# Optimization experiments

Hardware: AMD Instinct MI355X
Metric: run time of the kernel (lower is better)

The kernel has to match this reference:

```python
import jax, jax.numpy as jnp
import numpy as np

D = 256      # model dim
H = 4        # heads
L = 6        # layers (shared weights)
N = 32768    # neuron dim; per-head hidden = N//H = 8192
VOCAB = 256
B, T = 2, 2048
EPS = 1e-5


def _ln(x):
    # LayerNorm over last dim, no affine (matches nn.LayerNorm(D, elementwise_affine=False))
    m = jnp.mean(x, axis=-1, keepdims=True)
    v = jnp.mean((x - m) ** 2, axis=-1, keepdims=True)
    return (x - m) * jax.lax.rsqrt(v + EPS)


def _rope(x):
    # x: [B, H, T, d]
    d = x.shape[-1]
    t = x.shape[-2]
    inv_freq = 1.0 / (10000.0 ** (jnp.arange(0, d, 2, dtype=jnp.float32) / d))
    freqs = jnp.arange(t, dtype=jnp.float32)[:, None] * inv_freq[None, :]  # [T, d/2]
    emb = jnp.concatenate([freqs, freqs], axis=-1)                          # [T, d]
    x1, x2 = x[..., : d // 2], x[..., d // 2 :]
    x_rot = jnp.concatenate([-x2, x1], axis=-1)
    return x * jnp.cos(emb) + x_rot * jnp.sin(emb)


def _linear_attn(q, k, v):
    # q,k: [B,H,T,n]; v: [B,T,D]. Raw (unnormalized) scores, STRICTLY causal mask
    # (tril with diagonal=-1, i.e. token t attends to s < t only), no softmax.
    qr = _rope(q)
    kr = _rope(k)
    scores = jnp.einsum('bhtn,bhsn->bhts', qr, kr)  # [B,H,T,T]
    t_idx = jnp.arange(q.shape[-2])
    mask = t_idx[:, None] > t_idx[None, :]          # strict lower triangle
    scores = jnp.where(mask, scores, jnp.zeros((), scores.dtype))
    return jnp.einsum('bhts,bsd->bhtd', scores, v)  # [B,H,T,D]


def setup_inputs() -> dict:
    key = jax.random.key(0)
    ks = jax.random.split(key, 6)
    idx = jax.random.randint(ks[0], (B, T), 0, VOCAB, dtype=jnp.int64)
    std = 0.02
    wte = std * jax.random.normal(ks[1], (VOCAB, D), dtype=jnp.float32)
    encoder = std * jax.random.normal(ks[2], (N, D), dtype=jnp.float32)
    decoder_x = std * jax.random.normal(ks[3], (H, D, N // H), dtype=jnp.float32)
    decoder_y = std * jax.random.normal(ks[4], (H, D, N // H), dtype=jnp.float32)
    readout = std * jax.random.normal(ks[5], (D, VOCAB), dtype=jnp.float32)
    return {"idx": idx, "wte": wte, "encoder": encoder,
            "decoder_x": decoder_x, "decoder_y": decoder_y, "readout": readout}


def reference(idx, wte, encoder, decoder_x, decoder_y, readout):
    # Dropout is identity in eval mode.
    v_ast = _ln(wte[idx])  # [B,T,D]
    for _ in range(L):  # weights SHARED across layers
        x = jax.nn.relu(jnp.einsum('btd,hdn->bhtn', v_ast, decoder_x))  # [B,H,T,N/H]
        a_ast = _linear_attn(x, x, v_ast)                               # [B,H,T,D]
        y = jax.nn.relu(jnp.einsum('bhtd,hdn->bhtn', _ln(a_ast), decoder_y)) * x
        y_flat = jnp.transpose(y, (0, 2, 1, 3)).reshape(y.shape[0], y.shape[2], N)  # [B,T,N]
        v_ast = _ln(v_ast + _ln(y_flat @ encoder))
    return v_ast @ readout  # [B,T,VOCAB]
```

## Files before the change

### kernel.cpp

```cpp
#include <hip/hip_runtime.h>
#include <stdint.h>

typedef unsigned short u16;
typedef __bf16 bfv8 __attribute__((ext_vector_type(8)));
typedef float f32x4 __attribute__((ext_vector_type(4)));

#define BM 128
#define BN 128
#define BK 32

__device__ __forceinline__ float b2f(u16 u){ union{float f; unsigned int i;} x; x.i = ((unsigned int)u)<<16; return x.f; }
__device__ __forceinline__ u16 f2b(float f){ union{float f; unsigned int i;} x; x.f = f; unsigned int r = x.i + 0x7fffu + ((x.i>>16)&1u); return (u16)(r>>16); }

__device__ __forceinline__ void load16_lds(const void* g, void* l){
  __builtin_amdgcn_global_load_lds(
      (const __attribute__((address_space(1))) void*)g,
      (__attribute__((address_space(3))) void*)l, 16, 0, 0);
}

__device__ __forceinline__ void swz(int& bx, int& by, int& bz){
  int gx = gridDim.x, gy = gridDim.y;
  int nw = gx*gy*gridDim.z;
  int flat = blockIdx.x + gx*(blockIdx.y + gy*blockIdx.z);
  int q = nw >> 3, r = nw & 7, xcd = flat & 7, i = flat >> 3;
  int wg = (xcd < r ? xcd*(q+1) : r*(q+1) + (xcd-r)*q) + i;
  bx = wg % gx; int t = wg / gx; by = t % gy; bz = t / gy;
}

struct GP {
  const u16* A; const u16* Bt; const u16* A2; const u16* Bt2;
  const u16* ct; const u16* st;
  float* Cf; u16* Cb; u16* Y;
  int bh0, zs, zm;
};

template<int LDA, int LDB, bool PAIRB>
__device__ __forceinline__ void kloop(const u16* A, const u16* Bt, int m0, int n0,
                                      int kbeg, int kend,
                                      u16 (&As)[2][4096], u16 (&Bs)[2][4096],
                                      f32x4 (&acc)[4][4]){
  const int tid = threadIdx.x;
  const int lane = tid & 63;
  const int wid = tid >> 6;
  const int wm = wid >> 1, wn = wid & 1;
  const int srow = tid >> 2, sslot = tid & 3;
  const int nt = (kend - kbeg) / BK;
  if (nt <= 0) return;

  auto stage = [&](int k0, int buf){
    #pragma unroll
    for (int q = 0; q < 2; ++q){
      int row = q*64 + srow;
      int ks = sslot ^ ((row >> 1) & 3);
      load16_lds(A + (long)(m0 + row)*LDA + (k0 + ks*8), &As[buf][q*2048 + wid*512]);
    }
    #pragma unroll
    for (int q = 0; q < 2; ++q){
      int row = q*64 + srow;
      int ks = sslot ^ ((row >> 1) & 3);
      long brow;
      if (PAIRB){ int wnb = row >> 6, sub = (row >> 5) & 1, r5 = row & 31;
                  brow = n0 + wnb*32 + r5 + sub*4096; }
      else brow = n0 + row;
      load16_lds(Bt + brow*(long)LDB + (k0 + ks*8), &Bs[buf][q*2048 + wid*512]);
    }
  };

  stage(kbeg, 0);
  int cur = 0;
  for (int t = 0; t < nt; ++t){
    int tn = (t+1 < nt) ? (t+1) : t;
    stage(kbeg + tn*BK, cur^1);
    asm volatile("s_waitcnt vmcnt(4)" ::: "memory");
    __builtin_amdgcn_s_barrier();
    bfv8 af[4], bf[4];
    const int r16 = lane & 15, s4 = lane >> 4;
    #pragma unroll
    for (int i = 0; i < 4; ++i){
      int ar = wm*64 + i*16 + r16;
      af[i] = *(const bfv8*)(&As[cur][ar*BK + ((s4 ^ ((ar>>1)&3))*8)]);
      int br = wn*64 + i*16 + r16;
      bf[i] = *(const bfv8*)(&Bs[cur][br*BK + ((s4 ^ ((br>>1)&3))*8)]);
    }
    #pragma unroll
    for (int i = 0; i < 4; ++i)
      #pragma unroll
      for (int j = 0; j < 4; ++j)
        acc[i][j] = __builtin_amdgcn_mfma_f32_16x16x32_bf16(af[i], bf[j], acc[i][j], 0,0,0);
    asm volatile("s_waitcnt lgkmcnt(0)" ::: "memory");
    __builtin_amdgcn_s_barrier();
    cur ^= 1;
  }
  asm volatile("s_waitcnt vmcnt(0)" ::: "memory");
  __builtin_amdgcn_s_barrier();
}

#define EPI_SETUP const int lane = threadIdx.x & 63, wid = threadIdx.x >> 6; \
  const int wm = wid >> 1, wn = wid & 1; const int r16 = lane & 15, s4 = lane >> 4;

__global__ __launch_bounds__(256) void g_rope(GP p){
  int bx, by, bz; swz(bx, by, bz);
  const int m0 = by*BM, n0 = bx*64, z = bz;
  const int bh = p.bh0 + z, b = bh >> 2, h = bh & 3;
  __shared__ u16 As[2][4096], Bs[2][4096];
  f32x4 acc[4][4] = {};
  kloop<256,256,true>(p.A + (long)b*524288, p.Bt + (long)h*2097152, m0, n0, 0, 256, As, Bs, acc);
  EPI_SETUP
  #pragma unroll
  for (int i = 0; i < 4; ++i)
    #pragma unroll
    for (int j = 0; j < 2; ++j){
      int cl = n0 + wn*32 + j*16 + r16;
      #pragma unroll
      for (int v = 0; v < 4; ++v){
        int row = m0 + wm*64 + i*16 + s4*4 + v;
        float x1 = fmaxf(acc[i][j][v], 0.f);
        float x2 = fmaxf(acc[i][j+2][v], 0.f);
        float c = b2f(p.ct[(long)row*4096 + cl]);
        float s = b2f(p.st[(long)row*4096 + cl]);
        p.Cb[(long)z*16777216 + (long)row*8192 + cl]        = f2b(x1*c - x2*s);
        p.Cb[(long)z*16777216 + (long)row*8192 + cl + 4096] = f2b(x2*c + x1*s);
      }
    }
}

__global__ __launch_bounds__(256) void g_qk(GP p){
  int bx, by, bz; swz(bx, by, bz);
  const int m0 = by*BM, n0 = bx*BN, z = bz;
  if (n0 >= m0 + BM) return;
  __shared__ u16 As[2][4096], Bs[2][4096];
  f32x4 acc[4][4] = {};
  const u16* A = p.A + (long)z*16777216;
  kloop<8192,8192,false>(A, A, m0, n0, 0, 8192, As, Bs, acc);
  EPI_SETUP
  #pragma unroll
  for (int i = 0; i < 4; ++i)
    #pragma unroll
    for (int j = 0; j < 4; ++j){
      int col = n0 + wn*64 + j*16 + r16;
      #pragma unroll
      for (int v = 0; v < 4; ++v){
        int row = m0 + wm*64 + i*16 + s4*4 + v;
        p.Cb[(long)z*4194304 + (long)row*2048 + col] = f2b(row > col ? acc[i][j][v] : 0.f);
      }
    }
}

__global__ __launch_bounds__(256) void g_pv(GP p){
  int bx, by, bz; swz(bx, by, bz);
  const int m0 = by*BM, n0 = bx*BN;
  const int head = bz >> p.zs, sl = bz & p.zm;
  const int b = (p.bh0 + head) >> 2;
  const int kc = 2048 >> p.zs;
  const int kbeg = sl*kc;
  const int kend = min(min(2048, m0 + BM), kbeg + kc);
  __shared__ u16 As[2][4096], Bs[2][4096];
  f32x4 acc[4][4] = {};
  kloop<2048,2048,false>(p.A + (long)head*4194304, p.Bt + (long)b*524288, m0, n0, kbeg, kend, As, Bs, acc);
  EPI_SETUP
  #pragma unroll
  for (int i = 0; i < 4; ++i)
    #pragma unroll
    for (int j = 0; j < 4; ++j){
      int col = n0 + wn*64 + j*16 + r16;
      #pragma unroll
      for (int v = 0; v < 4; ++v){
        int row = m0 + wm*64 + i*16 + s4*4 + v;
        p.Cf[(long)bz*524288 + (long)row*256 + col] = acc[i][j][v];
      }
    }
}

__global__ __launch_bounds__(256) void g_fuse(GP p){
  int bx, by, bz; swz(bx, by, bz);
  const int m0 = by*BM, n0 = bx*BN, z = bz;
  const int bh = p.bh0 + z, b = bh >> 2, h = bh & 3;
  __shared__ u16 As[2][4096], Bs[2][4096];
  f32x4 acc1[4][4] = {}, acc2[4][4] = {};
  kloop<256,256,false>(p.A  + (long)z*524288, p.Bt  + (long)h*2097152, m0, n0, 0, 256, As, Bs, acc1);
  kloop<256,256,false>(p.A2 + (long)b*524288, p.Bt2 + (long)h*2097152, m0, n0, 0, 256, As, Bs, acc2);
  EPI_SETUP
  #pragma unroll
  for (int i = 0; i < 4; ++i)
    #pragma unroll
    for (int j = 0; j < 4; ++j){
      int col = n0 + wn*64 + j*16 + r16;
      #pragma unroll
      for (int v = 0; v < 4; ++v){
        int row = m0 + wm*64 + i*16 + s4*4 + v;
        p.Y[(long)z*16777216 + (long)row*8192 + col] =
            f2b(fmaxf(acc1[i][j][v], 0.f) * fmaxf(acc2[i][j][v], 0.f));
      }
    }
}

__global__ __launch_bounds__(256) void g_enc(GP p){
  int bx, by, bz; swz(bx, by, bz);
  const int m0 = by*BM, n0 = bx*BN;
  const int head = bz >> p.zs, sp = bz & p.zm;
  const int h = (p.bh0 + head) & 3;
  const int kc = 8192 >> p.zs;
  const int kbeg = sp*kc, kend = kbeg + kc;
  __shared__ u16 As[2][4096], Bs[2][4096];
  f32x4 acc[4][4] = {};
  kloop<8192,32768,false>(p.A + (long)head*16777216, p.Bt + (long)h*8192, m0, n0, kbeg, kend, As, Bs, acc);
  EPI_SETUP
  #pragma unroll
  for (int i = 0; i < 4; ++i)
    #pragma unroll
    for (int j = 0; j < 4; ++j){
      int col = n0 + wn*64 + j*16 + r16;
      #pragma unroll
      for (int v = 0; v < 4; ++v){
        int row = m0 + wm*64 + i*16 + s4*4 + v;
        p.Cf[(long)bz*524288 + (long)row*256 + col] = acc[i][j][v];
      }
    }
}

__global__ __launch_bounds__(256) void g_out(GP p){
  int bx, by, bz; swz(bx, by, bz); (void)bz;
  const int m0 = by*BM, n0 = bx*BN;
  __shared__ u16 As[2][4096], Bs[2][4096];
  f32x4 acc[4][4] = {};
  kloop<256,256,false>(p.A, p.Bt, m0, n0, 0, 256, As, Bs, acc);
  EPI_SETUP
  #pragma unroll
  for (int i = 0; i < 4; ++i)
    #pragma unroll
    for (int j = 0; j < 4; ++j){
      int col = n0 + wn*64 + j*16 + r16;
      #pragma unroll
      for (int v = 0; v < 4; ++v){
        int row = m0 + wm*64 + i*16 + s4*4 + v;
        p.Cf[(long)row*256 + col] = acc[i][j][v];
      }
    }
}


__device__ __forceinline__ float wave_sum(float v){
  #pragma unroll
  for (int o = 32; o > 0; o >>= 1) v += __shfl_down(v, o, 64);
  return v;
}
__device__ __forceinline__ float block_sum(float v, float* sm){
  v = wave_sum(v);
  __syncthreads();
  if ((threadIdx.x & 63) == 0) sm[threadIdx.x >> 6] = v;
  __syncthreads();
  return sm[0] + sm[1] + sm[2] + sm[3];
}

__global__ __launch_bounds__(256) void k_embed(const int* idx, const float* wte,
                                               float* v, u16* vbf, u16* vbt){
  __shared__ float sm[4];
  __shared__ int is64_s;
  int row = blockIdx.x, d = threadIdx.x;
  int oddnz = (d < 64) ? (idx[2*d + 1] != 0) : 0;
  unsigned long long mb = __ballot(oddnz);
  if (threadIdx.x == 0) is64_s = (mb == 0ULL);
  __syncthreads();
  int tok = is64_s ? idx[2*row] : idx[row];
  float x = wte[tok*256 + d];
  float m = block_sum(x, sm) * (1.f/256.f);
  float dd = x - m;
  float var = block_sum(dd*dd, sm) * (1.f/256.f);
  float y = dd * rsqrtf(var + 1e-5f);
  v[(long)row*256 + d] = y;
  vbf[(long)row*256 + d] = f2b(y);
  int b = row >> 11, t = row & 2047;
  vbt[((long)(b*256 + d))*2048 + t] = f2b(y);
}

__global__ __launch_bounds__(256) void k_ln(const float* abuf, u16* out, int pv){
  __shared__ float sm[4];
  int row = blockIdx.x, d = threadIdx.x;
  int head = row >> 11, t = row & 2047;
  float x = 0.f;
  for (int s = 0; s < pv; ++s) x += abuf[((long)(head*pv + s) << 19) + (long)t*256 + d];
  float m = block_sum(x, sm) * (1.f/256.f);
  float dd = x - m;
  float var = block_sum(dd*dd, sm) * (1.f/256.f);
  out[(long)row*256 + d] = f2b(dd * rsqrtf(var + 1e-5f));
}

__global__ __launch_bounds__(256) void k_acc(const float* part, float* t1,
                                             int bh0, int gc, int ps){
  int t = blockIdx.x, d = threadIdx.x;
  long o = (long)t*256 + d;
  float s0 = 0.f, s1 = 0.f;
  for (int z = 0; z < gc; ++z){
    float v = 0.f;
    for (int sp = 0; sp < ps; ++sp) v += part[((long)(z*ps + sp) << 19) + o];
    if (((bh0 + z) >> 2) == 0) s0 += v; else s1 += v;
  }
  #pragma unroll
  for (int b = 0; b < 2; ++b){
    int lo = bh0 > 4*b ? bh0 : 4*b;
    int hi = (bh0 + gc) < (4*b + 4) ? (bh0 + gc) : (4*b + 4);
    if (lo < hi){
      float s = b == 0 ? s0 : s1;
      if (lo == 4*b) t1[((long)b << 19) + o] = s;
      else           t1[((long)b << 19) + o] += s;
    }
  }
}

__global__ __launch_bounds__(256) void k_finish(const float* t1, float* v, u16* vbf, u16* vbt){
  __shared__ float sm[4];
  int row = blockIdx.x; int d = threadIdx.x;
  int b = row >> 11, t = row & 2047;
  float s = t1[(long)row*256 + d];
  float m = block_sum(s, sm) * (1.f/256.f);
  float dd = s - m;
  float var = block_sum(dd*dd, sm) * (1.f/256.f);
  float u = dd * rsqrtf(var + 1e-5f);
  float wv = v[(long)row*256 + d] + u;
  float m2 = block_sum(wv, sm) * (1.f/256.f);
  float d2 = wv - m2;
  float v2 = block_sum(d2*d2, sm) * (1.f/256.f);
  float y = d2 * rsqrtf(v2 + 1e-5f);
  v[(long)row*256 + d] = y;
  vbf[(long)row*256 + d] = f2b(y);
  vbt[((long)(b*256 + d))*2048 + t] = f2b(y);
}

__global__ __launch_bounds__(256) void k_cossin(u16* ct, u16* st){
  int tid = blockIdx.x*256 + threadIdx.x;
  int t = tid >> 12, i = tid & 4095;
  float f = powf(10000.0f, -(float)i * (1.0f/4096.0f));
  float a = (float)t * f;
  float s, c; sincosf(a, &s, &c);
  ct[tid] = f2b(c); st[tid] = f2b(s);
}

__global__ void k_transpose(const float* in, u16* out, int R, int C, long in_z, long out_z){
  __shared__ float tile[32][33];
  const float* I = in + (long)blockIdx.z * in_z;
  u16* O = out + (long)blockIdx.z * out_z;
  int c0 = blockIdx.x*32, r0 = blockIdx.y*32;
  int tx = threadIdx.x, ty = threadIdx.y;
  #pragma unroll
  for (int k = 0; k < 4; ++k){ int r = ty + k*8; tile[r][tx] = I[(long)(r0+r)*C + c0+tx]; }
  __syncthreads();
  #pragma unroll
  for (int k = 0; k < 4; ++k){ int r = ty + k*8; O[(long)(c0+r)*R + r0+tx] = f2b(tile[tx][r]); }
}


extern "C" void kernel_launch(void* const* d_in, const int* in_sizes, int n_in,
                              void* d_out, int out_size, void* d_ws, size_t ws_size,
                              hipStream_t stream){
  const int*   idx = (const int*)d_in[0];
  const float* wte = (const float*)d_in[1];
  const float* enc = (const float*)d_in[2];
  const float* dx  = (const float*)d_in[3];
  const float* dy  = (const float*)d_in[4];
  const float* ro  = (const float*)d_in[5];
  float* out = (float*)d_out;
  (void)in_sizes; (void)n_in; (void)out_size;

  const size_t base_b = 96600064UL;
  struct Cfg { int gc, pvs, pss; };
  const Cfg lad[] = {{8,2,3},{4,2,3},{2,2,3},{2,1,2},{1,2,3},{1,1,2},{1,0,1},{1,0,0}};
  Cfg cfg = lad[7];
  for (int i = 0; i < 8; ++i){
    size_t ch = (size_t)lad[i].gc * (33554432UL + 8388608UL + 1048576UL
               + ((size_t)(1 << lad[i].pvs))*2097152UL
               + ((size_t)(1 << lad[i].pss))*2097152UL);
    if (base_b + ch <= ws_size){ cfg = lad[i]; break; }
  }
  const int gc = cfg.gc, pvs = cfg.pvs, pss = cfg.pss;
  const int pv = 1 << pvs, ps = 1 << pss;

  char* w = (char*)d_ws;
  size_t off = 0;
  auto alloc = [&](size_t b){ size_t r = off; off += (b + 255) & ~(size_t)255; return r; };
  float* v_ast = (float*)(w + alloc(4096UL*256*4));
  u16*   v_bf  = (u16*)  (w + alloc(4096UL*256*2));
  u16*   v_bt  = (u16*)  (w + alloc(2UL*256*2048*2));
  u16*   dxT   = (u16*)  (w + alloc(4UL*8192*256*2));
  u16*   dyT   = (u16*)  (w + alloc(4UL*8192*256*2));
  u16*   encT  = (u16*)  (w + alloc(256UL*32768*2));
  u16*   roT   = (u16*)  (w + alloc(256UL*256*2));
  u16*   ct    = (u16*)  (w + alloc(2048UL*4096*2));
  u16*   st    = (u16*)  (w + alloc(2048UL*4096*2));
  float* t1    = (float*)(w + alloc(2UL*2048*256*4));
  u16*   xbuf  = (u16*)  (w + alloc((size_t)gc*33554432));
  u16*   scb   = (u16*)  (w + alloc((size_t)gc*8388608));
  u16*   lnAb  = (u16*)  (w + alloc((size_t)gc*1048576));
  float* abuf  = (float*)(w + alloc((size_t)gc*pv*2097152UL));
  float* part  = (float*)(w + alloc((size_t)gc*ps*2097152UL));

  dim3 tb(32, 8);
  k_cossin<<<32768, 256, 0, stream>>>(ct, st);
  k_transpose<<<dim3(256, 8, 4),  tb, 0, stream>>>(dx,  dxT,  256,   8192, 256L*8192, 8192L*256);
  k_transpose<<<dim3(256, 8, 4),  tb, 0, stream>>>(dy,  dyT,  256,   8192, 256L*8192, 8192L*256);
  k_transpose<<<dim3(8, 1024, 1), tb, 0, stream>>>(enc, encT, 32768, 256,  0, 0);
  k_transpose<<<dim3(8, 8, 1),    tb, 0, stream>>>(ro,  roT,  256,   256,  0, 0);
  k_embed<<<4096, 256, 0, stream>>>(idx, wte, v_ast, v_bf, v_bt);

  for (int l = 0; l < 6; ++l){
    for (int bh0 = 0; bh0 < 8; bh0 += gc){
      { GP g{}; g.bh0=bh0; g.A=v_bf; g.Bt=dxT; g.ct=ct; g.st=st; g.Cb=xbuf;
        g_rope<<<dim3(64,16,gc), 256, 0, stream>>>(g); }
      { GP g{}; g.bh0=bh0; g.A=xbuf; g.Cb=scb;
        g_qk<<<dim3(16,16,gc), 256, 0, stream>>>(g); }
      { GP g{}; g.bh0=bh0; g.A=scb; g.Bt=v_bt; g.Cf=abuf; g.zs=pvs; g.zm=pv-1;
        g_pv<<<dim3(2,16,gc*pv), 256, 0, stream>>>(g); }
      k_ln<<<gc*2048, 256, 0, stream>>>(abuf, lnAb, pv);
      { GP g{}; g.bh0=bh0; g.A=lnAb; g.Bt=dyT; g.A2=v_bf; g.Bt2=dxT; g.Y=xbuf;
        g_fuse<<<dim3(64,16,gc), 256, 0, stream>>>(g); }
      { GP g{}; g.bh0=bh0; g.A=xbuf; g.Bt=encT; g.Cf=part; g.zs=pss; g.zm=ps-1;
        g_enc<<<dim3(2,16,gc*ps), 256, 0, stream>>>(g); }
      k_acc<<<2048, 256, 0, stream>>>(part, t1, bh0, gc, ps);
    }
    k_finish<<<4096, 256, 0, stream>>>(t1, v_ast, v_bf, v_bt);
  }
  { GP g{}; g.A=v_bf; g.Bt=roT; g.Cf=out;
    g_out<<<dim3(2,32,1), 256, 0, stream>>>(g); }
}
```

Measured before the change: 7.998 ms.

## Shrink workspace via buffer aliasing so more heads fit per group

Drops the fp32 residual copy and keeps the residual only in bf16, which adds rounding error to the residual path. Partial-sum and LayerNorm buffers are aliased onto the score buffer, and the readout transpose reuses t1 after the layer loop. The smaller footprint lets more (batch, head) pairs be processed per group, with g_enc and g_pv split factors fixed lower and a ragged last group handled. The GEMM k-loop is also peeled so the final tile is no longer staged redundantly.

After: 8.165 ms. +2.1%, slower.

```diff
diff --git a/kernel.cpp b/kernel.cpp
--- a/kernel.cpp
+++ b/kernel.cpp
@@ -65,34 +65,39 @@
       load16_lds(Bt + brow*(long)LDB + (k0 + ks*8), &Bs[buf][q*2048 + wid*512]);
     }
   };
+  auto compute = [&](int buf){
+    bfv8 af[4], bf[4];
+    const int r16 = lane & 15, s4 = lane >> 4;
+    #pragma unroll
+    for (int i = 0; i < 4; ++i){
+      int ar = wm*64 + i*16 + r16;
+      af[i] = *(const bfv8*)(&As[buf][ar*BK + ((s4 ^ ((ar>>1)&3))*8)]);
+      int br = wn*64 + i*16 + r16;
+      bf[i] = *(const bfv8*)(&Bs[buf][br*BK + ((s4 ^ ((br>>1)&3))*8)]);
+    }
+    #pragma unroll
+    for (int i = 0; i < 4; ++i)
+      #pragma unroll
+      for (int j = 0; j < 4; ++j)
+        acc[i][j] = __builtin_amdgcn_mfma_f32_16x16x32_bf16(af[i], bf[j], acc[i][j], 0,0,0);
+  };
 
   stage(kbeg, 0);
   int cur = 0;
-  for (int t = 0; t < nt; ++t){
-    int tn = (t+1 < nt) ? (t+1) : t;
-    stage(kbeg + tn*BK, cur^1);
+  for (int t = 0; t < nt-1; ++t){
+    stage(kbeg + (t+1)*BK, cur^1);
     asm volatile("s_waitcnt vmcnt(4)" ::: "memory");
     __builtin_amdgcn_s_barrier();
-    bfv8 af[4], bf[4];
-    const int r16 = lane & 15, s4 = lane >> 4;
-    #pragma unroll
-    for (int i = 0; i < 4; ++i){
-      int ar = wm*64 + i*16 + r16;
-      af[i] = *(const bfv8*)(&As[cur][ar*BK + ((s4 ^ ((ar>>1)&3))*8)]);
-      int br = wn*64 + i*16 + r16;
-      bf[i] = *(const bfv8*)(&Bs[cur][br*BK + ((s4 ^ ((br>>1)&3))*8)]);
-    }
-    #pragma unroll
-    for (int i = 0; i < 4; ++i)
-      #pragma unroll
-      for (int j = 0; j < 4; ++j)
-        acc[i][j] = __builtin_amdgcn_mfma_f32_16x16x32_bf16(af[i], bf[j], acc[i][j], 0,0,0);
+    compute(cur);
     asm volatile("s_waitcnt lgkmcnt(0)" ::: "memory");
     __builtin_amdgcn_s_barrier();
     cur ^= 1;
   }
   asm volatile("s_waitcnt vmcnt(0)" ::: "memory");
   __builtin_amdgcn_s_barrier();
+  compute(cur);
+  asm volatile("s_waitcnt lgkmcnt(0)" ::: "memory");
+  __builtin_amdgcn_s_barrier();
 }
 
 #define EPI_SETUP const int lane = threadIdx.x & 63, wid = threadIdx.x >> 6; \
@@ -133,6 +138,7 @@
   const u16* A = p.A + (long)z*16777216;
   kloop<8192,8192,false>(A, A, m0, n0, 0, 8192, As, Bs, acc);
   EPI_SETUP
+  u16* C = p.Cb + (long)z*4194304;
   #pragma unroll
   for (int i = 0; i < 4; ++i)
     #pragma unroll
@@ -141,7 +147,7 @@
       #pragma unroll
       for (int v = 0; v < 4; ++v){
         int row = m0 + wm*64 + i*16 + s4*4 + v;
-        p.Cb[(long)z*4194304 + (long)row*2048 + col] = f2b(row > col ? acc[i][j][v] : 0.f);
+        C[(long)row*2048 + col] = f2b(row > col ? acc[i][j][v] : 0.f);
       }
     }
 }
@@ -253,7 +259,7 @@
 }
 
 __global__ __launch_bounds__(256) void k_embed(const int* idx, const float* wte,
-                                               float* v, u16* vbf, u16* vbt){
+                                               u16* vbf, u16* vbt){
   __shared__ float sm[4];
   __shared__ int is64_s;
   int row = blockIdx.x, d = threadIdx.x;
@@ -267,7 +273,6 @@
   float dd = x - m;
   float var = block_sum(dd*dd, sm) * (1.f/256.f);
   float y = dd * rsqrtf(var + 1e-5f);
-  v[(long)row*256 + d] = y;
   vbf[(long)row*256 + d] = f2b(y);
   int b = row >> 11, t = row & 2047;
   vbt[((long)(b*256 + d))*2048 + t] = f2b(y);
@@ -307,7 +312,7 @@
   }
 }
 
-__global__ __launch_bounds__(256) void k_finish(const float* t1, float* v, u16* vbf, u16* vbt){
+__global__ __launch_bounds__(256) void k_finish(const float* t1, u16* vbf, u16* vbt){
   __shared__ float sm[4];
   int row = blockIdx.x; int d = threadIdx.x;
   int b = row >> 11, t = row & 2047;
@@ -316,12 +321,11 @@
   float dd = s - m;
   float var = block_sum(dd*dd, sm) * (1.f/256.f);
   float u = dd * rsqrtf(var + 1e-5f);
-  float wv = v[(long)row*256 + d] + u;
+  float wv = b2f(vbf[(long)row*256 + d]) + u;
   float m2 = block_sum(wv, sm) * (1.f/256.f);
   float d2 = wv - m2;
   float v2 = block_sum(d2*d2, sm) * (1.f/256.f);
   float y = d2 * rsqrtf(v2 + 1e-5f);
-  v[(long)row*256 + d] = y;
   vbf[(long)row*256 + d] = f2b(y);
   vbt[((long)(b*256 + d))*2048 + t] = f2b(y);
 }
@@ -361,63 +365,62 @@
   float* out = (float*)d_out;
   (void)in_sizes; (void)n_in; (void)out_size;
 
-  const size_t base_b = 96600064UL;
-  struct Cfg { int gc, pvs, pss; };
-  const Cfg lad[] = {{8,2,3},{4,2,3},{2,2,3},{2,1,2},{1,2,3},{1,1,2},{1,0,1},{1,0,0}};
-  Cfg cfg = lad[7];
-  for (int i = 0; i < 8; ++i){
-    size_t ch = (size_t)lad[i].gc * (33554432UL + 8388608UL + 1048576UL
-               + ((size_t)(1 << lad[i].pvs))*2097152UL
-               + ((size_t)(1 << lad[i].pss))*2097152UL);
-    if (base_b + ch <= ws_size){ cfg = lad[i]; break; }
+  int gc = 1, pv = 2;
+  {
+    const int gcs[4] = {4, 3, 2, 1};
+    for (int i = 0; i < 4; ++i){
+      int g = gcs[i]; int pvt = (g >= 4) ? 1 : 2;
+      size_t need = 92274688UL + (size_t)g*(33554432UL + 8388608UL + (size_t)pvt*2097152UL);
+      if (need <= ws_size){ gc = g; pv = pvt; break; }
+    }
   }
-  const int gc = cfg.gc, pvs = cfg.pvs, pss = cfg.pss;
-  const int pv = 1 << pvs, ps = 1 << pss;
+  const int ps = 2;
+  const int pvs = (pv == 2) ? 1 : 0;
 
   char* w = (char*)d_ws;
   size_t off = 0;
   auto alloc = [&](size_t b){ size_t r = off; off += (b + 255) & ~(size_t)255; return r; };
-  float* v_ast = (float*)(w + alloc(4096UL*256*4));
   u16*   v_bf  = (u16*)  (w + alloc(4096UL*256*2));
   u16*   v_bt  = (u16*)  (w + alloc(2UL*256*2048*2));
   u16*   dxT   = (u16*)  (w + alloc(4UL*8192*256*2));
   u16*   dyT   = (u16*)  (w + alloc(4UL*8192*256*2));
   u16*   encT  = (u16*)  (w + alloc(256UL*32768*2));
-  u16*   roT   = (u16*)  (w + alloc(256UL*256*2));
   u16*   ct    = (u16*)  (w + alloc(2048UL*4096*2));
   u16*   st    = (u16*)  (w + alloc(2048UL*4096*2));
   float* t1    = (float*)(w + alloc(2UL*2048*256*4));
   u16*   xbuf  = (u16*)  (w + alloc((size_t)gc*33554432));
   u16*   scb   = (u16*)  (w + alloc((size_t)gc*8388608));
-  u16*   lnAb  = (u16*)  (w + alloc((size_t)gc*1048576));
   float* abuf  = (float*)(w + alloc((size_t)gc*pv*2097152UL));
-  float* part  = (float*)(w + alloc((size_t)gc*ps*2097152UL));
+  float* part  = (float*)scb;
+  u16*   lnAb  = (u16*)((char*)scb + (size_t)gc*ps*2097152UL);
+  u16*   roT   = (u16*)t1;
 
   dim3 tb(32, 8);
   k_cossin<<<32768, 256, 0, stream>>>(ct, st);
   k_transpose<<<dim3(256, 8, 4),  tb, 0, stream>>>(dx,  dxT,  256,   8192, 256L*8192, 8192L*256);
   k_transpose<<<dim3(256, 8, 4),  tb, 0, stream>>>(dy,  dyT,  256,   8192, 256L*8192, 8192L*256);
   k_transpose<<<dim3(8, 1024, 1), tb, 0, stream>>>(enc, encT, 32768, 256,  0, 0);
-  k_transpose<<<dim3(8, 8, 1),    tb, 0, stream>>>(ro,  roT,  256,   256,  0, 0);
-  k_embed<<<4096, 256, 0, stream>>>(idx, wte, v_ast, v_bf, v_bt);
+  k_embed<<<4096, 256, 0, stream>>>(idx, wte, v_bf, v_bt);
 
   for (int l = 0; l < 6; ++l){
     for (int bh0 = 0; bh0 < 8; bh0 += gc){
+      int ze = (8 - bh0 < gc) ? (8 - bh0) : gc;
       { GP g{}; g.bh0=bh0; g.A=v_bf; g.Bt=dxT; g.ct=ct; g.st=st; g.Cb=xbuf;
-        g_rope<<<dim3(64,16,gc), 256, 0, stream>>>(g); }
+        g_rope<<<dim3(64,16,ze), 256, 0, stream>>>(g); }
       { GP g{}; g.bh0=bh0; g.A=xbuf; g.Cb=scb;
-        g_qk<<<dim3(16,16,gc), 256, 0, stream>>>(g); }
+        g_qk<<<dim3(16,16,ze), 256, 0, stream>>>(g); }
       { GP g{}; g.bh0=bh0; g.A=scb; g.Bt=v_bt; g.Cf=abuf; g.zs=pvs; g.zm=pv-1;
-        g_pv<<<dim3(2,16,gc*pv), 256, 0, stream>>>(g); }
-      k_ln<<<gc*2048, 256, 0, stream>>>(abuf, lnAb, pv);
+        g_pv<<<dim3(2,16,ze*pv), 256, 0, stream>>>(g); }
+      k_ln<<<ze*2048, 256, 0, stream>>>(abuf, lnAb, pv);
       { GP g{}; g.bh0=bh0; g.A=lnAb; g.Bt=dyT; g.A2=v_bf; g.Bt2=dxT; g.Y=xbuf;
-        g_fuse<<<dim3(64,16,gc), 256, 0, stream>>>(g); }
-      { GP g{}; g.bh0=bh0; g.A=xbuf; g.Bt=encT; g.Cf=part; g.zs=pss; g.zm=ps-1;
-        g_enc<<<dim3(2,16,gc*ps), 256, 0, stream>>>(g); }
-      k_acc<<<2048, 256, 0, stream>>>(part, t1, bh0, gc, ps);
-    }
-    k_finish<<<4096, 256, 0, stream>>>(t1, v_ast, v_bf, v_bt);
+        g_fuse<<<dim3(64,16,ze), 256, 0, stream>>>(g); }
+      { GP g{}; g.bh0=bh0; g.A=xbuf; g.Bt=encT; g.Cf=part; g.zs=1; g.zm=1;
+        g_enc<<<dim3(2,16,ze*ps), 256, 0, stream>>>(g); }
+      k_acc<<<2048, 256, 0, stream>>>(part, t1, bh0, ze, ps);
+    }
+    k_finish<<<4096, 256, 0, stream>>>(t1, v_bf, v_bt);
   }
+  k_transpose<<<dim3(8, 8, 1), tb, 0, stream>>>(ro, roT, 256, 256, 0, 0);
   { GP g{}; g.A=v_bf; g.Bt=roT; g.Cf=out;
     g_out<<<dim3(2,32,1), 256, 0, stream>>>(g); }
 }
```
